# Performance work log

Measured on AMD Instinct MI355X. Metric: run time of the kernel, lower is better.

The kernel has to match this reference:

```python
import jax, jax.numpy as jnp
import numpy as np

N_NODES = 100000


def gcn_conv(x, W, b, src, dst, dinv):
    # PyG GCNConv with default add_self_loops=True, symmetric normalization.
    # x: [N, Fin], W: [Fin, Fout]. Self-loop contribution handled analytically
    # (norm for loop edge i->i is dinv[i]^2) instead of materializing loop edges.
    xw = x @ W                                   # [N, Fout]
    norm = dinv[src] * dinv[dst]                 # [E]
    msgs = xw[src] * norm[:, None]               # [E, Fout]
    agg = jax.ops.segment_sum(msgs, dst, num_segments=N_NODES)
    agg = agg + xw * (dinv * dinv)[:, None]      # self-loops
    return agg + b


def setup_inputs() -> dict:
    key = jax.random.key(0)
    ks = jax.random.split(key, 12)
    E = 3200000
    S = 1000000
    F_in = 512
    x = jax.random.normal(ks[0], (N_NODES, F_in), dtype=jnp.float32)
    edge_index = jax.random.randint(ks[1], (2, E), 0, N_NODES, dtype=jnp.int64)
    samples = jax.random.randint(ks[2], (S, 2), 0, N_NODES, dtype=jnp.int64)

    def glorot(k, fi, fo):
        lim = float(np.sqrt(6.0 / (fi + fo)))
        return jax.random.uniform(k, (fi, fo), jnp.float32, -lim, lim)

    W1 = glorot(ks[3], F_in, 8)
    b1 = jnp.zeros((8,), jnp.float32)
    W2 = glorot(ks[4], 8, 16)
    b2 = jnp.zeros((16,), jnp.float32)
    W3 = glorot(ks[5], 16, 32)
    b3 = jnp.zeros((32,), jnp.float32)
    Wfc = glorot(ks[6], 64, 1)
    bfc = jnp.zeros((1,), jnp.float32)
    return {"x": x, "edge_index": edge_index, "samples": samples,
            "W1": W1, "b1": b1, "W2": W2, "b2": b2, "W3": W3, "b3": b3,
            "Wfc": Wfc, "bfc": bfc}


def reference(x, edge_index, samples, W1, b1, W2, b2, W3, b3, Wfc, bfc):
    src, dst = edge_index[0], edge_index[1]
    # degree with self-loops (edge weight 1), deg >= 1 so rsqrt is safe
    deg = jax.ops.segment_sum(jnp.ones_like(src, dtype=x.dtype), dst,
                              num_segments=N_NODES) + 1.0
    dinv = jax.lax.rsqrt(deg)
    h = jax.nn.relu(gcn_conv(x, W1, b1, src, dst, dinv))
    h = jax.nn.relu(gcn_conv(h, W2, b2, src, dst, dinv))
    h = gcn_conv(h, W3, b3, src, dst, dinv)
    x_i = h[samples[:, 0]]                       # [S, 32]
    x_j = h[samples[:, 1]]                       # [S, 32]
    x_ij = jnp.concatenate([x_i, x_j], axis=1)   # [S, 64]
    return jax.nn.sigmoid(x_ij @ Wfc + bfc).squeeze(-1)
```

## Files before the change

kernel.cpp:

```cpp
#include <hip/hip_runtime.h>
#include <cstdint>

#define N_NODES 100000
#define NBKT 2048
#define KNODE 49
#define NBLK 256
#define TPB_P 512


__global__ void k_hist(const int* __restrict__ dst, int* __restrict__ hist, int E) {
    __shared__ int h[NBKT];
    for (int i = threadIdx.x; i < NBKT; i += blockDim.x) h[i] = 0;
    __syncthreads();
    int chunk = (E + NBLK - 1) / NBLK;
    int lo = blockIdx.x * chunk, hi = min(lo + chunk, E);
    for (int i = lo + threadIdx.x; i < hi; i += blockDim.x)
        atomicAdd(&h[dst[i] / KNODE], 1);
    __syncthreads();
    int* hr = hist + (size_t)blockIdx.x * NBKT;
    for (int i = threadIdx.x; i < NBKT; i += blockDim.x) hr[i] = h[i];
}


__global__ void k_offs(const int* __restrict__ hist, int* __restrict__ offs,
                       int* __restrict__ btot) {
    int bkt = blockIdx.x * blockDim.x + threadIdx.x;
    if (bkt >= NBKT) return;
    int run = 0;
    for (int rr = 0; rr < NBLK; ++rr) {
        int r = ((rr & 31) << 3) | (rr >> 5);
        int v = hist[(size_t)r * NBKT + bkt];
        offs[(size_t)r * NBKT + bkt] = run;
        run += v;
    }
    btot[bkt] = run;
}


__global__ void k_bktscan(const int* __restrict__ btot, int* __restrict__ bbase) {
    __shared__ int s[256];
    int t = threadIdx.x;
    int loc[8];
    int sum = 0;
#pragma unroll
    for (int j = 0; j < 8; ++j) { loc[j] = btot[t * 8 + j]; sum += loc[j]; }
    s[t] = sum;
    __syncthreads();
    for (int off = 1; off < 256; off <<= 1) {
        int v = (t >= off) ? s[t - off] : 0;
        __syncthreads();
        s[t] += v;
        __syncthreads();
    }
    int base = s[t] - sum;
#pragma unroll
    for (int j = 0; j < 8; ++j) { bbase[t * 8 + j] = base; base += loc[j]; }
    if (t == 255) bbase[NBKT] = base;
}


__global__ void k_place(const int* __restrict__ src, const int* __restrict__ dst,
                        const int* __restrict__ offs, const int* __restrict__ bbase,
                        int* __restrict__ tmp, int E) {
    __shared__ int cur[NBKT];
    const int* orow = offs + (size_t)blockIdx.x * NBKT;
    for (int i = threadIdx.x; i < NBKT; i += blockDim.x) cur[i] = bbase[i] + orow[i];
    __syncthreads();
    int chunk = (E + NBLK - 1) / NBLK;
    int lo = blockIdx.x * chunk, hi = min(lo + chunk, E);
    for (int i = lo + threadIdx.x; i < hi; i += blockDim.x) {
        int d = dst[i], s = src[i];
        int b = d / KNODE;
        int p = atomicAdd(&cur[b], 1);
        tmp[p] = (s << 6) | (d - b * KNODE);
    }
}


__global__ void k_countscan(const int* __restrict__ tmp, const int* __restrict__ bbase,
                            int* __restrict__ row_start, float* __restrict__ dinv, int n) {
    __shared__ int c[KNODE];
    __shared__ int p[KNODE];
    int b = blockIdx.x;
    int t = threadIdx.x;
    for (int i = t; i < KNODE; i += blockDim.x) c[i] = 0;
    __syncthreads();
    int n0 = bbase[b], n1 = bbase[b + 1];
    for (int i = n0 + t; i < n1; i += blockDim.x)
        atomicAdd(&c[tmp[i] & 63], 1);
    __syncthreads();
    if (t == 0) {
        int run = 0;
        for (int j = 0; j < KNODE; ++j) { p[j] = run; run += c[j]; }
    }
    __syncthreads();
    if (t < KNODE) {
        int node = b * KNODE + t;
        if (node < n) {
            row_start[node] = n0 + p[t];
            dinv[node] = rsqrtf((float)c[t] + 1.0f);
        }
    }
    if (b == 0 && t == 0) row_start[n] = bbase[NBKT];
}


__global__ void k_bin2(const int* __restrict__ tmp, const int* __restrict__ bbase,
                       const int* __restrict__ row_start, const float* __restrict__ dinv,
                       int2* __restrict__ csr, int n) {
    __shared__ int cur[KNODE];
    __shared__ float dd[KNODE];
    int b = blockIdx.x;
    int t = threadIdx.x;
    if (t < KNODE) {
        int node = b * KNODE + t;
        cur[t] = (node < n) ? row_start[node] : 0;
        dd[t] = (node < n) ? dinv[node] : 0.f;
    }
    __syncthreads();
    int n0 = bbase[b], n1 = bbase[b + 1];
    for (int i = n0 + t; i < n1; i += blockDim.x) {
        int e = tmp[i];
        int li = e & 63;
        int s = e >> 6;
        int pos = atomicAdd(&cur[li], 1);
        csr[pos] = make_int2(s, __float_as_int(dinv[s] * dd[li]));
    }
}


__global__ void k_gemm1(const float* __restrict__ x, const float* __restrict__ W,
                        float* __restrict__ xw, int n) {
    __shared__ float sW[512 * 8];
    for (int i = threadIdx.x; i < 512 * 8; i += blockDim.x) sW[i] = W[i];
    __syncthreads();
    int r = blockIdx.x * blockDim.x + threadIdx.x;
    if (r >= n) return;
    const float4* xr = (const float4*)(x + (size_t)r * 512);
    float acc[8];
#pragma unroll
    for (int c = 0; c < 8; ++c) acc[c] = 0.f;
    for (int t = 0; t < 128; ++t) {
        float4 v = xr[t];
        const float* sw = &sW[t * 32];
#pragma unroll
        for (int c = 0; c < 8; ++c)
            acc[c] += v.x * sw[c] + v.y * sw[8 + c] + v.z * sw[16 + c] + v.w * sw[24 + c];
    }
    float4* xwo = (float4*)(xw + (size_t)r * 8);
    xwo[0] = make_float4(acc[0], acc[1], acc[2], acc[3]);
    xwo[1] = make_float4(acc[4], acc[5], acc[6], acc[7]);
}


template <int FIN, int FOUT, bool RELU>
__global__ void k_gemm_small(const float* __restrict__ h, const float* __restrict__ W,
                             const float* __restrict__ b, float* __restrict__ xw, int n) {
    __shared__ float sW[FIN * FOUT];
    __shared__ float sB[FOUT];
    for (int i = threadIdx.x; i < FIN * FOUT; i += blockDim.x) sW[i] = W[i];
    for (int i = threadIdx.x; i < FOUT; i += blockDim.x) sB[i] = b[i];
    __syncthreads();
    int r = blockIdx.x * blockDim.x + threadIdx.x;
    if (r >= n) return;
    float in[FIN];
    const float4* hp = (const float4*)(h + (size_t)r * FIN);
#pragma unroll
    for (int t = 0; t < FIN / 4; ++t) {
        float4 v = hp[t];
        in[t * 4 + 0] = v.x; in[t * 4 + 1] = v.y; in[t * 4 + 2] = v.z; in[t * 4 + 3] = v.w;
    }
    float4* xwo = (float4*)(xw + (size_t)r * FOUT);
#pragma unroll
    for (int c = 0; c < FOUT; c += 4) {
        float s[4];
#pragma unroll
        for (int j = 0; j < 4; ++j) {
            float a = 0.f;
#pragma unroll
            for (int k = 0; k < FIN; ++k) a += in[k] * sW[k * FOUT + c + j];
            a += sB[c + j];
            if (RELU) a = fmaxf(a, 0.f);
            s[j] = a;
        }
        xwo[c / 4] = make_float4(s[0], s[1], s[2], s[3]);
    }
}


template <int F, bool FIN_BIAS_RELU>
__global__ void k_gather(const float* __restrict__ xw, const int2* __restrict__ csr,
                         const int* __restrict__ row_start, const float* __restrict__ dinv,
                         const float* __restrict__ b, float* __restrict__ out, int n) {
    int gid = blockIdx.x * blockDim.x + threadIdx.x;
    int node = gid / F;
    int c = gid % F;
    if (node >= n) return;
    float di = dinv[node];
    float acc = xw[(size_t)node * F + c] * di * di;
    int k0 = row_start[node], k1 = row_start[node + 1];
    for (int k = k0; k < k1; ++k) {
        int2 p = csr[k];
        acc += xw[(size_t)p.x * F + c] * __int_as_float(p.y);
    }
    if (FIN_BIAS_RELU) acc = fmaxf(acc + b[c], 0.f);
    out[(size_t)node * F + c] = acc;
}


__global__ void k_prep_head(const float* __restrict__ W3, const float* __restrict__ b3,
                            const float* __restrict__ Wfc, float* __restrict__ v,
                            float* __restrict__ c) {
    int t = threadIdx.x;
    if (t < 32) {
        int j = t & 15;
        const float* wf = Wfc + (t < 16 ? 0 : 32);
        float a = 0.f;
        for (int k = 0; k < 32; ++k) a += W3[j * 32 + k] * wf[k];
        v[t] = a;
    } else if (t < 34) {
        const float* wf = Wfc + (t == 32 ? 0 : 32);
        float a = 0.f;
        for (int k = 0; k < 32; ++k) a += b3[k] * wf[k];
        c[t - 32] = a;
    }
}

__global__ void k_node_head(const float* __restrict__ S3, const float* __restrict__ v,
                            const float* __restrict__ c, float* __restrict__ pi,
                            float* __restrict__ pj, int n) {
    int r = blockIdx.x * blockDim.x + threadIdx.x;
    if (r >= n) return;
    const float4* sp = (const float4*)(S3 + (size_t)r * 16);
    float a = 0.f, bb = 0.f;
#pragma unroll
    for (int t = 0; t < 4; ++t) {
        float4 s = sp[t];
        a += s.x * v[t * 4 + 0] + s.y * v[t * 4 + 1] + s.z * v[t * 4 + 2] + s.w * v[t * 4 + 3];
        bb += s.x * v[16 + t * 4 + 0] + s.y * v[16 + t * 4 + 1] + s.z * v[16 + t * 4 + 2] + s.w * v[16 + t * 4 + 3];
    }
    pi[r] = a + c[0];
    pj[r] = bb + c[1];
}


__global__ void k_samples_fast(const int2* __restrict__ samples, const float* __restrict__ pi,
                               const float* __restrict__ pj, const float* __restrict__ bfc,
                               float* __restrict__ out, int S) {
    int i = blockIdx.x * blockDim.x + threadIdx.x;
    if (i >= S) return;
    int2 s = samples[i];
    float z = pi[s.x] + pj[s.y] + bfc[0];
    out[i] = 1.0f / (1.0f + __expf(-z));
}


extern "C" void kernel_launch(void* const* d_in, const int* in_sizes, int n_in,
                              void* d_out, int out_size, void* d_ws, size_t ws_size,
                              hipStream_t stream) {
    const float* x   = (const float*)d_in[0];
    const int*   ei  = (const int*)d_in[1];
    const int*   smp = (const int*)d_in[2];
    const float* W1  = (const float*)d_in[3];
    const float* b1  = (const float*)d_in[4];
    const float* W2  = (const float*)d_in[5];
    const float* b2  = (const float*)d_in[6];
    const float* W3  = (const float*)d_in[7];
    const float* b3  = (const float*)d_in[8];
    const float* Wfc = (const float*)d_in[9];
    const float* bfc = (const float*)d_in[10];
    float* out = (float*)d_out;

    const int E = in_sizes[1] / 2;
    const int S = in_sizes[2] / 2;
    const int N = N_NODES;
    const int* src = ei;
    const int* dst = ei + E;

    char* w = (char*)d_ws;
    size_t off = 0;
    auto alloc = [&](size_t bytes) {
        char* p = w + off;
        off += (bytes + 255) & ~(size_t)255;
        return p;
    };
    int*   row_start = (int*)alloc((N + 1) * 4);
    float* dinv      = (float*)alloc(N * 4);
    int2*  csr       = (int2*)alloc((size_t)E * 8);
    int*   btot      = (int*)alloc(NBKT * 4);
    int*   bbase     = (int*)alloc((NBKT + 1) * 4);

    size_t off_layers = off;
    float* xw1       = (float*)alloc((size_t)N * 8 * 4);
    float* h1        = (float*)alloc((size_t)N * 8 * 4);
    float* S2        = (float*)alloc((size_t)N * 8 * 4);
    float* h2        = (float*)alloc((size_t)N * 16 * 4);
    float* S3        = (float*)alloc((size_t)N * 16 * 4);
    float* vhead     = (float*)alloc(32 * 4);
    float* chead     = (float*)alloc(2 * 4);
    float* pi        = (float*)alloc(N * 4);
    float* pj        = (float*)alloc(N * 4);

    size_t tmp_off  = off_layers;
    size_t hist_off = tmp_off + (((size_t)E * 4 + 255) & ~(size_t)255);
    size_t offs_off = hist_off + (((size_t)NBLK * NBKT * 4 + 255) & ~(size_t)255);
    int* tmp  = (int*)(w + tmp_off);
    int* hist = (int*)(w + hist_off);
    int* offs = (int*)(w + offs_off);
    size_t scratch_end = offs_off + (size_t)NBLK * NBKT * 4;
    if (scratch_end > off) off = (scratch_end + 255) & ~(size_t)255;

    dim3 B(256);

    k_hist<<<dim3(NBLK), dim3(TPB_P), 0, stream>>>(dst, hist, E);
    k_offs<<<dim3((NBKT + 255) / 256), B, 0, stream>>>(hist, offs, btot);
    k_bktscan<<<dim3(1), B, 0, stream>>>(btot, bbase);
    k_place<<<dim3(NBLK), dim3(TPB_P), 0, stream>>>(src, dst, offs, bbase, tmp, E);
    k_countscan<<<dim3(NBKT), B, 0, stream>>>(tmp, bbase, row_start, dinv, N);
    k_bin2<<<dim3(NBKT), B, 0, stream>>>(tmp, bbase, row_start, dinv, csr, N);

    k_gemm1<<<dim3((N + 255) / 256), B, 0, stream>>>(x, W1, xw1, N);
    k_gather<8, true><<<dim3(((size_t)N * 8 + 255) / 256), B, 0, stream>>>(xw1, csr, row_start, dinv, b1, h1, N);

    k_gather<8, false><<<dim3(((size_t)N * 8 + 255) / 256), B, 0, stream>>>(h1, csr, row_start, dinv, nullptr, S2, N);
    k_gemm_small<8, 16, true><<<dim3((N + 255) / 256), B, 0, stream>>>(S2, W2, b2, h2, N);

    k_gather<16, false><<<dim3(((size_t)N * 16 + 255) / 256), B, 0, stream>>>(h2, csr, row_start, dinv, nullptr, S3, N);

    k_prep_head<<<dim3(1), dim3(64), 0, stream>>>(W3, b3, Wfc, vhead, chead);
    k_node_head<<<dim3((N + 255) / 256), B, 0, stream>>>(S3, vhead, chead, pi, pj, N);
    k_samples_fast<<<dim3((S + 255) / 256), B, 0, stream>>>((const int2*)smp, pi, pj, bfc, out, S);
}
```

Before: 639.3 us.

## Use wave-per-node gathers, fuse small GEMM and head into aggregation kernels

```diff
diff --git a/kernel.cpp b/kernel.cpp
--- a/kernel.cpp
+++ b/kernel.cpp
@@ -131,80 +131,122 @@
 
 __global__ void k_gemm1(const float* __restrict__ x, const float* __restrict__ W,
                         float* __restrict__ xw, int n) {
-    __shared__ float sW[512 * 8];
-    for (int i = threadIdx.x; i < 512 * 8; i += blockDim.x) sW[i] = W[i];
-    __syncthreads();
-    int r = blockIdx.x * blockDim.x + threadIdx.x;
-    if (r >= n) return;
-    const float4* xr = (const float4*)(x + (size_t)r * 512);
+    __shared__ float sWT[8 * 512];
+    for (int i = threadIdx.x; i < 4096; i += blockDim.x) {
+        int k = i >> 3, c = i & 7;
+        sWT[c * 512 + k] = W[i];
+    }
+    __syncthreads();
+    int wid = (blockIdx.x * blockDim.x + threadIdx.x) >> 6;
+    int lane = threadIdx.x & 63;
+    int r_sub = lane >> 3, j = lane & 7;
+    int row = wid * 8 + r_sub;
+    if (row >= n) return;
+    const float* xr = x + (size_t)row * 512;
     float acc[8];
 #pragma unroll
     for (int c = 0; c < 8; ++c) acc[c] = 0.f;
-    for (int t = 0; t < 128; ++t) {
-        float4 v = xr[t];
-        const float* sw = &sW[t * 32];
+#pragma unroll 4
+    for (int it = 0; it < 16; ++it) {
+        int kb = it * 32 + j * 4;
+        float4 v = *(const float4*)(xr + kb);
+#pragma unroll
+        for (int c = 0; c < 8; ++c) {
+            const float* wt = &sWT[c * 512 + kb];
+            acc[c] += v.x * wt[0] + v.y * wt[1] + v.z * wt[2] + v.w * wt[3];
+        }
+    }
+#pragma unroll
+    for (int off = 1; off < 8; off <<= 1)
 #pragma unroll
         for (int c = 0; c < 8; ++c)
-            acc[c] += v.x * sw[c] + v.y * sw[8 + c] + v.z * sw[16 + c] + v.w * sw[24 + c];
-    }
-    float4* xwo = (float4*)(xw + (size_t)r * 8);
-    xwo[0] = make_float4(acc[0], acc[1], acc[2], acc[3]);
-    xwo[1] = make_float4(acc[4], acc[5], acc[6], acc[7]);
-}
-
-
-template <int FIN, int FOUT, bool RELU>
-__global__ void k_gemm_small(const float* __restrict__ h, const float* __restrict__ W,
-                             const float* __restrict__ b, float* __restrict__ xw, int n) {
-    __shared__ float sW[FIN * FOUT];
-    __shared__ float sB[FOUT];
-    for (int i = threadIdx.x; i < FIN * FOUT; i += blockDim.x) sW[i] = W[i];
-    for (int i = threadIdx.x; i < FOUT; i += blockDim.x) sB[i] = b[i];
-    __syncthreads();
-    int r = blockIdx.x * blockDim.x + threadIdx.x;
-    if (r >= n) return;
-    float in[FIN];
-    const float4* hp = (const float4*)(h + (size_t)r * FIN);
-#pragma unroll
-    for (int t = 0; t < FIN / 4; ++t) {
-        float4 v = hp[t];
-        in[t * 4 + 0] = v.x; in[t * 4 + 1] = v.y; in[t * 4 + 2] = v.z; in[t * 4 + 3] = v.w;
-    }
-    float4* xwo = (float4*)(xw + (size_t)r * FOUT);
-#pragma unroll
-    for (int c = 0; c < FOUT; c += 4) {
-        float s[4];
-#pragma unroll
-        for (int j = 0; j < 4; ++j) {
-            float a = 0.f;
-#pragma unroll
-            for (int k = 0; k < FIN; ++k) a += in[k] * sW[k * FOUT + c + j];
-            a += sB[c + j];
-            if (RELU) a = fmaxf(a, 0.f);
-            s[j] = a;
-        }
-        xwo[c / 4] = make_float4(s[0], s[1], s[2], s[3]);
-    }
-}
-
-
-template <int F, bool FIN_BIAS_RELU>
-__global__ void k_gather(const float* __restrict__ xw, const int2* __restrict__ csr,
-                         const int* __restrict__ row_start, const float* __restrict__ dinv,
-                         const float* __restrict__ b, float* __restrict__ out, int n) {
-    int gid = blockIdx.x * blockDim.x + threadIdx.x;
-    int node = gid / F;
-    int c = gid % F;
-    if (node >= n) return;
-    float di = dinv[node];
-    float acc = xw[(size_t)node * F + c] * di * di;
-    int k0 = row_start[node], k1 = row_start[node + 1];
-    for (int k = k0; k < k1; ++k) {
+            acc[c] += __shfl_xor(acc[c], off);
+    float outv = acc[0];
+#pragma unroll
+    for (int c = 1; c < 8; ++c) if (j == c) outv = acc[c];
+    xw[(size_t)row * 8 + j] = outv;
+}
+
+
+__global__ void k_gather1(const float* __restrict__ xw, const int2* __restrict__ csr,
+                          const int* __restrict__ row_start, const float* __restrict__ dinv,
+                          const float* __restrict__ b, float* __restrict__ out, int n) {
+    int wid = (blockIdx.x * blockDim.x + threadIdx.x) >> 6;
+    int lane = threadIdx.x & 63;
+    if (wid >= n) return;
+    int e = lane >> 3, c = lane & 7;
+    int k0 = row_start[wid], k1 = row_start[wid + 1];
+    float acc = 0.f;
+    for (int k = k0 + e; k < k1; k += 8) {
         int2 p = csr[k];
-        acc += xw[(size_t)p.x * F + c] * __int_as_float(p.y);
-    }
-    if (FIN_BIAS_RELU) acc = fmaxf(acc + b[c], 0.f);
-    out[(size_t)node * F + c] = acc;
+        acc += xw[(size_t)p.x * 8 + c] * __int_as_float(p.y);
+    }
+    if (e == 0) { float di = dinv[wid]; acc += xw[(size_t)wid * 8 + c] * di * di; }
+#pragma unroll
+    for (int off = 8; off < 64; off <<= 1) acc += __shfl_xor(acc, off);
+    if (lane < 8) out[(size_t)wid * 8 + c] = fmaxf(acc + b[c], 0.f);
+}
+
+
+__global__ void k_gather2(const float* __restrict__ h1, const int2* __restrict__ csr,
+                          const int* __restrict__ row_start, const float* __restrict__ dinv,
+                          const float* __restrict__ W2, const float* __restrict__ b2,
+                          float* __restrict__ h2, int n) {
+    __shared__ float sW[8 * 16];
+    __shared__ float sB[16];
+    if (threadIdx.x < 128) sW[threadIdx.x] = W2[threadIdx.x];
+    if (threadIdx.x < 16) sB[threadIdx.x] = b2[threadIdx.x];
+    __syncthreads();
+    int wid = (blockIdx.x * blockDim.x + threadIdx.x) >> 6;
+    int lane = threadIdx.x & 63;
+    if (wid >= n) return;
+    int e = lane >> 3, c = lane & 7;
+    int k0 = row_start[wid], k1 = row_start[wid + 1];
+    float acc = 0.f;
+    for (int k = k0 + e; k < k1; k += 8) {
+        int2 p = csr[k];
+        acc += h1[(size_t)p.x * 8 + c] * __int_as_float(p.y);
+    }
+    if (e == 0) { float di = dinv[wid]; acc += h1[(size_t)wid * 8 + c] * di * di; }
+#pragma unroll
+    for (int off = 8; off < 64; off <<= 1) acc += __shfl_xor(acc, off);
+    float s2[8];
+#pragma unroll
+    for (int k = 0; k < 8; ++k) s2[k] = __shfl(acc, k);
+    if (lane < 16) {
+        float a = sB[lane];
+#pragma unroll
+        for (int k = 0; k < 8; ++k) a += s2[k] * sW[k * 16 + lane];
+        h2[(size_t)wid * 16 + lane] = fmaxf(a, 0.f);
+    }
+}
+
+
+__global__ void k_gather3(const float* __restrict__ h2, const int2* __restrict__ csr,
+                          const int* __restrict__ row_start, const float* __restrict__ dinv,
+                          const float* __restrict__ v, const float* __restrict__ ch,
+                          float* __restrict__ pi, float* __restrict__ pj, int n) {
+    int wid = (blockIdx.x * blockDim.x + threadIdx.x) >> 6;
+    int lane = threadIdx.x & 63;
+    if (wid >= n) return;
+    int e = lane >> 4, c = lane & 15;
+    int k0 = row_start[wid], k1 = row_start[wid + 1];
+    float acc = 0.f;
+    for (int k = k0 + e; k < k1; k += 4) {
+        int2 p = csr[k];
+        acc += h2[(size_t)p.x * 16 + c] * __int_as_float(p.y);
+    }
+    if (e == 0) { float di = dinv[wid]; acc += h2[(size_t)wid * 16 + c] * di * di; }
+#pragma unroll
+    for (int off = 16; off < 64; off <<= 1) acc += __shfl_xor(acc, off);
+    float t = acc * v[c];
+    float u = acc * v[16 + c];
+#pragma unroll
+    for (int off = 1; off < 16; off <<= 1) {
+        t += __shfl_xor(t, off);
+        u += __shfl_xor(u, off);
+    }
+    if (lane == 0) { pi[wid] = t + ch[0]; pj[wid] = u + ch[1]; }
 }
 
 
@@ -226,23 +268,6 @@
     }
 }
 
-__global__ void k_node_head(const float* __restrict__ S3, const float* __restrict__ v,
-                            const float* __restrict__ c, float* __restrict__ pi,
-                            float* __restrict__ pj, int n) {
-    int r = blockIdx.x * blockDim.x + threadIdx.x;
-    if (r >= n) return;
-    const float4* sp = (const float4*)(S3 + (size_t)r * 16);
-    float a = 0.f, bb = 0.f;
-#pragma unroll
-    for (int t = 0; t < 4; ++t) {
-        float4 s = sp[t];
-        a += s.x * v[t * 4 + 0] + s.y * v[t * 4 + 1] + s.z * v[t * 4 + 2] + s.w * v[t * 4 + 3];
-        bb += s.x * v[16 + t * 4 + 0] + s.y * v[16 + t * 4 + 1] + s.z * v[16 + t * 4 + 2] + s.w * v[16 + t * 4 + 3];
-    }
-    pi[r] = a + c[0];
-    pj[r] = bb + c[1];
-}
-
 
 __global__ void k_samples_fast(const int2* __restrict__ samples, const float* __restrict__ pi,
                                const float* __restrict__ pj, const float* __restrict__ bfc,
@@ -293,9 +318,7 @@
     size_t off_layers = off;
     float* xw1       = (float*)alloc((size_t)N * 8 * 4);
     float* h1        = (float*)alloc((size_t)N * 8 * 4);
-    float* S2        = (float*)alloc((size_t)N * 8 * 4);
     float* h2        = (float*)alloc((size_t)N * 16 * 4);
-    float* S3        = (float*)alloc((size_t)N * 16 * 4);
     float* vhead     = (float*)alloc(32 * 4);
     float* chead     = (float*)alloc(2 * 4);
     float* pi        = (float*)alloc(N * 4);
@@ -311,6 +334,7 @@
     if (scratch_end > off) off = (scratch_end + 255) & ~(size_t)255;
 
     dim3 B(256);
+    const int GN = (N * 64 + 255) / 256;
 
     k_hist<<<dim3(NBLK), dim3(TPB_P), 0, stream>>>(dst, hist, E);
     k_offs<<<dim3((NBKT + 255) / 256), B, 0, stream>>>(hist, offs, btot);
@@ -319,15 +343,13 @@
     k_countscan<<<dim3(NBKT), B, 0, stream>>>(tmp, bbase, row_start, dinv, N);
     k_bin2<<<dim3(NBKT), B, 0, stream>>>(tmp, bbase, row_start, dinv, csr, N);
 
-    k_gemm1<<<dim3((N + 255) / 256), B, 0, stream>>>(x, W1, xw1, N);
-    k_gather<8, true><<<dim3(((size_t)N * 8 + 255) / 256), B, 0, stream>>>(xw1, csr, row_start, dinv, b1, h1, N);
-
-    k_gather<8, false><<<dim3(((size_t)N * 8 + 255) / 256), B, 0, stream>>>(h1, csr, row_start, dinv, nullptr, S2, N);
-    k_gemm_small<8, 16, true><<<dim3((N + 255) / 256), B, 0, stream>>>(S2, W2, b2, h2, N);
-
-    k_gather<16, false><<<dim3(((size_t)N * 16 + 255) / 256), B, 0, stream>>>(h2, csr, row_start, dinv, nullptr, S3, N);
+    k_gemm1<<<dim3(((N + 7) / 8 * 64 + 255) / 256), B, 0, stream>>>(x, W1, xw1, N);
+    k_gather1<<<dim3(GN), B, 0, stream>>>(xw1, csr, row_start, dinv, b1, h1, N);
+
+    k_gather2<<<dim3(GN), B, 0, stream>>>(h1, csr, row_start, dinv, W2, b2, h2, N);
 
     k_prep_head<<<dim3(1), dim3(64), 0, stream>>>(W3, b3, Wfc, vhead, chead);
-    k_node_head<<<dim3((N + 255) / 256), B, 0, stream>>>(S3, vhead, chead, pi, pj, N);
+    k_gather3<<<dim3(GN), B, 0, stream>>>(h2, csr, row_start, dinv, vhead, chead, pi, pj, N);
+
     k_samples_fast<<<dim3((S + 255) / 256), B, 0, stream>>>((const int2*)smp, pi, pj, bfc, out, S);
 }
```

Result: no change. 638.4 us (-0.1%).
